# Optimization experiments

Measured on AMD Instinct MI355X. Metric: run time of the kernel, lower is better.

## Reference

```python
import jax, jax.numpy as jnp
import numpy as np

B = 262144
I = 128  # input_size
H = 128  # hidden_size


def setup_inputs() -> dict:
    key = jax.random.key(0)
    ks = jax.random.split(key, 12)
    std = 1.0 / np.sqrt(H)
    u = lambda k, shape: jax.random.uniform(k, shape, jnp.float32, -std, std)
    return {
        "inputs": jax.random.normal(ks[0], (B, I), jnp.float32),
        "h_prev": jax.random.normal(ks[1], (B, H), jnp.float32),
        "c_prev": jax.random.normal(ks[2], (B, H), jnp.float32),
        "W_ii": u(ks[3], (H, I)), "W_hi": u(ks[4], (H, H)),
        "W_if": u(ks[5], (H, I)), "W_hf": u(ks[6], (H, H)),
        "W_io": u(ks[7], (H, I)), "W_ho": u(ks[8], (H, H)),
        "W_ig": u(ks[9], (H, I)), "W_hg": u(ks[10], (H, H)),
    }


def reference(inputs, h_prev, c_prev, W_ii, W_hi, W_if, W_hf, W_io, W_ho, W_ig, W_hg):
    # Same math as 8 separate GEMMs, expressed as 2 fused GEMMs over concatenated gates.
    W_x = jnp.concatenate([W_ii, W_if, W_io, W_ig], axis=0)  # [4H, I]
    W_h = jnp.concatenate([W_hi, W_hf, W_ho, W_hg], axis=0)  # [4H, H]
    gates = inputs @ W_x.T + h_prev @ W_h.T  # [B, 4H]
    gi, gf, go, gg = jnp.split(gates, 4, axis=-1)
    i_t = jax.nn.sigmoid(gi)
    f_t = jax.nn.sigmoid(gf)
    o_t = jax.nn.sigmoid(go)
    g_t = jnp.tanh(gg)
    c_t = f_t * c_prev + i_t * g_t
    h_t = o_t * jnp.tanh(c_t)
    return jnp.stack([h_t, c_t], axis=0)  # [2, B, H]
```

## Files before the change

### kernel.cpp

```cpp
#include <hip/hip_runtime.h>

#define BATCH 262144
#define NBLK 256
#define NITER 16
#define ASTRIDE 264
#define BH 33554432

typedef __attribute__((ext_vector_type(8))) short bf16x8;
typedef __attribute__((ext_vector_type(4))) float f32x4;
typedef __attribute__((ext_vector_type(8))) unsigned short u16x8;

__device__ __forceinline__ unsigned short f2bf(float f) {
  unsigned int u = __float_as_uint(f);
  u += 0x7fffu + ((u >> 16) & 1u);
  return (unsigned short)(u >> 16);
}

__device__ __forceinline__ float fexp(float x) { return __builtin_amdgcn_exp2f(x * 1.44269504f); }
__device__ __forceinline__ float sigm(float x) { return __builtin_amdgcn_rcpf(1.f + fexp(-x)); }
__device__ __forceinline__ float ftanh(float x) { return 1.f - 2.f * __builtin_amdgcn_rcpf(1.f + fexp(2.f * x)); }

__global__ __launch_bounds__(512, 2) void lstm_fused(
    const float* __restrict__ X, const float* __restrict__ H0, const float* __restrict__ C0,
    const float* __restrict__ Wii, const float* __restrict__ Whi,
    const float* __restrict__ Wif, const float* __restrict__ Whf,
    const float* __restrict__ Wio, const float* __restrict__ Who,
    const float* __restrict__ Wig, const float* __restrict__ Whg,
    float* __restrict__ Out) {
  __shared__ __align__(16) unsigned short Abuf[64 * ASTRIDE];

  const int tid = threadIdx.x;
  const int wave = tid >> 6;
  const int lane = tid & 63;
  const int lrow = lane & 15;
  const int lk = (lane >> 4) * 8;
  const int hcol = wave * 16 + lrow;

  const float* Wxp[4] = {Wii, Wif, Wio, Wig};
  const float* Whp[4] = {Whi, Whf, Who, Whg};

  bf16x8 wf[4][8];
#pragma unroll
  for (int g = 0; g < 4; ++g) {
#pragma unroll
    for (int kk = 0; kk < 8; ++kk) {
      const int k = kk * 32 + lk;
      const float* src = (kk < 4) ? (Wxp[g] + hcol * 128 + k)
                                  : (Whp[g] + hcol * 128 + (k - 128));
      float4 lo = *(const float4*)src;
      float4 hi = *(const float4*)(src + 4);
      bf16x8 w;
      w[0] = (short)f2bf(lo.x); w[1] = (short)f2bf(lo.y);
      w[2] = (short)f2bf(lo.z); w[3] = (short)f2bf(lo.w);
      w[4] = (short)f2bf(hi.x); w[5] = (short)f2bf(hi.y);
      w[6] = (short)f2bf(hi.z); w[7] = (short)f2bf(hi.w);
      wf[g][kk] = w;
    }
  }

  float4 sx[4], sh[4];

  auto issue_loads = [&](int row0) {
#pragma unroll
    for (int j = 0; j < 2; ++j) {
      const int f = tid + j * 512;
      const int r = f >> 4;
      const int c = (f & 15) * 8;
      const float* px = X + (size_t)(row0 + r) * 128 + c;
      sx[j * 2 + 0] = *(const float4*)px;
      sx[j * 2 + 1] = *(const float4*)(px + 4);
      const float* ph = H0 + (size_t)(row0 + r) * 128 + c;
      sh[j * 2 + 0] = *(const float4*)ph;
      sh[j * 2 + 1] = *(const float4*)(ph + 4);
    }
  };

  issue_loads(blockIdx.x * 64);

  for (int it = 0; it < NITER; ++it) {
    const int tile = blockIdx.x + it * NBLK;
    const int row0 = tile * 64;

    __syncthreads();

#pragma unroll
    for (int j = 0; j < 2; ++j) {
      const int f = tid + j * 512;
      const int r = f >> 4;
      const int c = (f & 15) * 8;
      u16x8 w;
      w[0] = f2bf(sx[j * 2].x);     w[1] = f2bf(sx[j * 2].y);
      w[2] = f2bf(sx[j * 2].z);     w[3] = f2bf(sx[j * 2].w);
      w[4] = f2bf(sx[j * 2 + 1].x); w[5] = f2bf(sx[j * 2 + 1].y);
      w[6] = f2bf(sx[j * 2 + 1].z); w[7] = f2bf(sx[j * 2 + 1].w);
      *(u16x8*)&Abuf[r * ASTRIDE + c] = w;
      u16x8 v;
      v[0] = f2bf(sh[j * 2].x);     v[1] = f2bf(sh[j * 2].y);
      v[2] = f2bf(sh[j * 2].z);     v[3] = f2bf(sh[j * 2].w);
      v[4] = f2bf(sh[j * 2 + 1].x); v[5] = f2bf(sh[j * 2 + 1].y);
      v[6] = f2bf(sh[j * 2 + 1].z); v[7] = f2bf(sh[j * 2 + 1].w);
      *(u16x8*)&Abuf[r * ASTRIDE + 128 + c] = v;
    }

    if (it + 1 < NITER) issue_loads(row0 + NBLK * 64);

    __syncthreads();

    const int rb = row0 + (lane >> 4) * 4;
    float cv[16];
#pragma unroll
    for (int mt = 0; mt < 4; ++mt)
#pragma unroll
      for (int j = 0; j < 4; ++j)
        cv[mt * 4 + j] = C0[(size_t)(rb + mt * 16 + j) * 128 + hcol];

#pragma unroll
    for (int mt = 0; mt < 4; ++mt) {
      f32x4 acc0 = {0.f, 0.f, 0.f, 0.f};
      f32x4 acc1 = acc0, acc2 = acc0, acc3 = acc0;
#pragma unroll
      for (int kk = 0; kk < 8; ++kk) {
        bf16x8 a = *(const bf16x8*)&Abuf[(mt * 16 + lrow) * ASTRIDE + kk * 32 + lk];
        acc0 = __builtin_amdgcn_mfma_f32_16x16x32_bf16(a, wf[0][kk], acc0, 0, 0, 0);
        acc1 = __builtin_amdgcn_mfma_f32_16x16x32_bf16(a, wf[1][kk], acc1, 0, 0, 0);
        acc2 = __builtin_amdgcn_mfma_f32_16x16x32_bf16(a, wf[2][kk], acc2, 0, 0, 0);
        acc3 = __builtin_amdgcn_mfma_f32_16x16x32_bf16(a, wf[3][kk], acc3, 0, 0, 0);
      }
      const int rbase = rb + mt * 16;
#pragma unroll
      for (int j = 0; j < 4; ++j) {
        const int rg = rbase + j;
        const float cprev = cv[mt * 4 + j];
        const float it_ = sigm(acc0[j]);
        const float ft = sigm(acc1[j]);
        const float ot = sigm(acc2[j]);
        const float gt = ftanh(acc3[j]);
        const float ct = ft * cprev + it_ * gt;
        const float ht = ot * ftanh(ct);
        Out[(size_t)rg * 128 + hcol] = ht;
        Out[BH + (size_t)rg * 128 + hcol] = ct;
      }
    }
  }
}

extern "C" void kernel_launch(void* const* d_in, const int* in_sizes, int n_in,
                              void* d_out, int out_size, void* d_ws, size_t ws_size,
                              hipStream_t stream) {
  (void)in_sizes; (void)n_in; (void)out_size; (void)d_ws; (void)ws_size;
  lstm_fused<<<NBLK, 512, 0, stream>>>(
      (const float*)d_in[0], (const float*)d_in[1], (const float*)d_in[2],
      (const float*)d_in[3], (const float*)d_in[4], (const float*)d_in[5],
      (const float*)d_in[6], (const float*)d_in[7], (const float*)d_in[8],
      (const float*)d_in[9], (const float*)d_in[10],
      (float*)d_out);
}
```

Before: 156.5 us.

## Double-buffer LDS tile and prefetch next c_prev to drop a barrier

Splits the shared A buffer into two halves used alternately, which removes one __syncthreads per iteration. The c_prev loads for the next tile are now issued one iteration early, so their latency overlaps the MFMA work. The loop is manually unrolled by two so the buffer and register sets can be swapped. In exchange, LDS use doubles (about 67KB per block), and the extra 16 live registers may affect occupancy at 2 blocks per CU.

```diff
diff --git a/kernel.cpp b/kernel.cpp
--- a/kernel.cpp
+++ b/kernel.cpp
@@ -27,7 +27,7 @@
     const float* __restrict__ Wio, const float* __restrict__ Who,
     const float* __restrict__ Wig, const float* __restrict__ Whg,
     float* __restrict__ Out) {
-  __shared__ __align__(16) unsigned short Abuf[64 * ASTRIDE];
+  __shared__ __align__(16) unsigned short Abuf[2][64 * ASTRIDE];
 
   const int tid = threadIdx.x;
   const int wave = tid >> 6;
@@ -75,13 +75,19 @@
     }
   };
 
-  issue_loads(blockIdx.x * 64);
+  auto issue_cv = [&](int row0, float (&cv)[16]) {
+    const int rb = row0 + (lane >> 4) * 4;
+#pragma unroll
+    for (int mt = 0; mt < 4; ++mt)
+#pragma unroll
+      for (int j = 0; j < 4; ++j)
+        cv[mt * 4 + j] = C0[(size_t)(rb + mt * 16 + j) * 128 + hcol];
+  };
 
-  for (int it = 0; it < NITER; ++it) {
-    const int tile = blockIdx.x + it * NBLK;
-    const int row0 = tile * 64;
+  float cv0[16], cv1[16];
 
-    __syncthreads();
+  auto body = [&](int it, unsigned short* ab, float (&cvR)[16], float (&cvW)[16]) {
+    const int row0 = (blockIdx.x + it * NBLK) * 64;
 
 #pragma unroll
     for (int j = 0; j < 2; ++j) {
@@ -93,34 +99,31 @@
       w[2] = f2bf(sx[j * 2].z);     w[3] = f2bf(sx[j * 2].w);
       w[4] = f2bf(sx[j * 2 + 1].x); w[5] = f2bf(sx[j * 2 + 1].y);
       w[6] = f2bf(sx[j * 2 + 1].z); w[7] = f2bf(sx[j * 2 + 1].w);
-      *(u16x8*)&Abuf[r * ASTRIDE + c] = w;
+      *(u16x8*)&ab[r * ASTRIDE + c] = w;
       u16x8 v;
       v[0] = f2bf(sh[j * 2].x);     v[1] = f2bf(sh[j * 2].y);
       v[2] = f2bf(sh[j * 2].z);     v[3] = f2bf(sh[j * 2].w);
       v[4] = f2bf(sh[j * 2 + 1].x); v[5] = f2bf(sh[j * 2 + 1].y);
       v[6] = f2bf(sh[j * 2 + 1].z); v[7] = f2bf(sh[j * 2 + 1].w);
-      *(u16x8*)&Abuf[r * ASTRIDE + 128 + c] = v;
+      *(u16x8*)&ab[r * ASTRIDE + 128 + c] = v;
     }
-
-    if (it + 1 < NITER) issue_loads(row0 + NBLK * 64);
 
     __syncthreads();
 
+    if (it + 1 < NITER) {
+      const int nrow0 = row0 + NBLK * 64;
+      issue_loads(nrow0);
+      issue_cv(nrow0, cvW);
+    }
+
     const int rb = row0 + (lane >> 4) * 4;
-    float cv[16];
-#pragma unroll
-    for (int mt = 0; mt < 4; ++mt)
-#pragma unroll
-      for (int j = 0; j < 4; ++j)
-        cv[mt * 4 + j] = C0[(size_t)(rb + mt * 16 + j) * 128 + hcol];
-
 #pragma unroll
     for (int mt = 0; mt < 4; ++mt) {
       f32x4 acc0 = {0.f, 0.f, 0.f, 0.f};
       f32x4 acc1 = acc0, acc2 = acc0, acc3 = acc0;
 #pragma unroll
       for (int kk = 0; kk < 8; ++kk) {
-        bf16x8 a = *(const bf16x8*)&Abuf[(mt * 16 + lrow) * ASTRIDE + kk * 32 + lk];
+        bf16x8 a = *(const bf16x8*)&ab[(mt * 16 + lrow) * ASTRIDE + kk * 32 + lk];
         acc0 = __builtin_amdgcn_mfma_f32_16x16x32_bf16(a, wf[0][kk], acc0, 0, 0, 0);
         acc1 = __builtin_amdgcn_mfma_f32_16x16x32_bf16(a, wf[1][kk], acc1, 0, 0, 0);
         acc2 = __builtin_amdgcn_mfma_f32_16x16x32_bf16(a, wf[2][kk], acc2, 0, 0, 0);
@@ -130,7 +133,7 @@
 #pragma unroll
       for (int j = 0; j < 4; ++j) {
         const int rg = rbase + j;
-        const float cprev = cv[mt * 4 + j];
+        const float cprev = cvR[mt * 4 + j];
         const float it_ = sigm(acc0[j]);
         const float ft = sigm(acc1[j]);
         const float ot = sigm(acc2[j]);
@@ -141,6 +144,15 @@
         Out[BH + (size_t)rg * 128 + hcol] = ct;
       }
     }
+  };
+
+  const int row00 = blockIdx.x * 64;
+  issue_loads(row00);
+  issue_cv(row00, cv0);
+
+  for (int it = 0; it < NITER; it += 2) {
+    body(it, &Abuf[0][0], cv0, cv1);
+    body(it + 1, &Abuf[1][0], cv1, cv0);
   }
 }
 
```

New measurement: 583.2 us. +272.6%, slower.
